# Kernel tuning notes

Measured on AMD Instinct MI355X. Metric: run time of the kernel, lower is better.

The kernel has to match this reference:

```python
import jax, jax.numpy as jnp
import numpy as np

B, S, H, E = 2, 4096, 2048, 8


def setup_inputs() -> dict:
    key = jax.random.key(0)
    k1, k2, k3 = jax.random.split(key, 3)
    x = jax.random.normal(k1, (B, S, H), dtype=jnp.float32)
    w_router = jax.random.normal(k2, (E, H), dtype=jnp.float32) * (1.0 / np.sqrt(H))
    # nn.Linear weight layout: [out_features, in_features] per expert -> [E, H, H]
    w_experts = jax.random.normal(k3, (E, H, H), dtype=jnp.float32) * (1.0 / np.sqrt(H))
    return {"x": x, "w_router": w_router, "w_experts": w_experts}


def reference(x, w_router, w_experts):
    # router logits: x @ W_r^T  -> [B, S, E]
    logits = jnp.einsum('bsh,eh->bse', x, w_router)
    idx = jnp.argmax(logits, axis=-1)  # [B, S] top-1 expert per token
    # dense all-expert outputs (matches original which evaluates every expert):
    # expert_e(x) = x @ W_e^T -> [B, S, E, H]
    all_out = jnp.einsum('bsh,efh->bsef', x, w_experts)
    # masked sum over one-hot mask == gather of the selected expert output
    out = jnp.take_along_axis(all_out, idx[:, :, None, None], axis=2)[:, :, 0, :]
    return out
```

## Files before the change

kernel.cpp:

```cpp
#include <hip/hip_runtime.h>
#include <hip/hip_bf16.h>
#include <cstdint>

#define T_TOK 8192
#define H_DIM 2048
#define N_EXP 8
#define FLAGBIT 0x80000000u

typedef __attribute__((ext_vector_type(4))) float f32x4;
typedef __attribute__((ext_vector_type(8))) short bf16x8;

__device__ __forceinline__ unsigned short f2bf(float f) {
  unsigned int u = __builtin_bit_cast(unsigned int, f);
  u += 0x7fffu + ((u >> 16) & 1u);
  return (unsigned short)(u >> 16);
}

#define GLL(SRC, DST) __builtin_amdgcn_global_load_lds( \
    (const __attribute__((address_space(1))) void*)(SRC), \
    (__attribute__((address_space(3))) void*)(DST), 16, 0, 0)

__global__ __launch_bounds__(256, 4) void k_pre(const float* __restrict__ x,
    const float* __restrict__ wr, const float* __restrict__ we,
    unsigned short* __restrict__ xb, unsigned short* __restrict__ wb,
    int* __restrict__ idx)
{
  const int bid = blockIdx.x;
  if (bid < 4096) {
    const size_t tix = ((size_t)bid * 256 + threadIdx.x) * 8;
    const size_t stride = (size_t)4096 * 256 * 8;
#pragma unroll
    for (int it = 0; it < 4; ++it) {
      const f32x4 a = *reinterpret_cast<const f32x4*>(we + tix + (size_t)it * stride);
      const f32x4 b = *reinterpret_cast<const f32x4*>(we + tix + (size_t)it * stride + 4);
      union { unsigned short h[8]; uint4 u; } r;
#pragma unroll
      for (int q = 0; q < 4; ++q) { r.h[q] = f2bf(a[q]); r.h[4 + q] = f2bf(b[q]); }
      *reinterpret_cast<uint4*>(wb + tix + (size_t)it * stride) = r.u;
    }
    return;
  }
  const int wv = threadIdx.x >> 6, lane = threadIdx.x & 63;
  const int t = (bid - 4096) * 4 + wv;
  const float* xp = x + (size_t)t * H_DIM;
  float acc[N_EXP];
#pragma unroll
  for (int e = 0; e < N_EXP; ++e) acc[e] = 0.f;
#pragma unroll
  for (int c = 0; c < H_DIM / 256; ++c) {
    const int h = c * 256 + lane * 4;
    const float4 xv = *reinterpret_cast<const float4*>(xp + h);
    ushort4 bv;
    bv.x = f2bf(xv.x); bv.y = f2bf(xv.y); bv.z = f2bf(xv.z); bv.w = f2bf(xv.w);
    *reinterpret_cast<ushort4*>(xb + (size_t)t * H_DIM + h) = bv;
#pragma unroll
    for (int e = 0; e < N_EXP; ++e) {
      const float4 wv4 = *reinterpret_cast<const float4*>(wr + e * H_DIM + h);
      acc[e] = fmaf(xv.x, wv4.x, acc[e]);
      acc[e] = fmaf(xv.y, wv4.y, acc[e]);
      acc[e] = fmaf(xv.z, wv4.z, acc[e]);
      acc[e] = fmaf(xv.w, wv4.w, acc[e]);
    }
  }
#pragma unroll
  for (int off = 32; off >= 1; off >>= 1)
#pragma unroll
    for (int e = 0; e < N_EXP; ++e) acc[e] += __shfl_xor(acc[e], off, 64);
  if (lane == 0) {
    float best = acc[0]; int be = 0;
#pragma unroll
    for (int e = 1; e < N_EXP; ++e) if (acc[e] > best) { best = acc[e]; be = e; }
    idx[t] = be;
  }
}

__global__ __launch_bounds__(1024) void k_sort(const int* __restrict__ idx,
    int* __restrict__ tlist, int* __restrict__ estar, int* __restrict__ mlo,
    int* __restrict__ mhi, int* __restrict__ rpos, int* __restrict__ rtile,
    int* __restrict__ rtc)
{
  __shared__ int wc[N_EXP][128];
  __shared__ int wbase[N_EXP][128];
  __shared__ int sTot[N_EXP];
  __shared__ int off[N_EXP + 1];
  __shared__ int sE[32], sCnt[N_EXP], sBase[N_EXP];
  const int tid = threadIdx.x, w = tid >> 6, l = tid & 63;
  int myE[8];
#pragma unroll
  for (int j = 0; j < 8; ++j) {
    myE[j] = idx[j * 1024 + tid];
#pragma unroll
    for (int e = 0; e < N_EXP; ++e) {
      const unsigned long long bm = __ballot(myE[j] == e);
      if (l == e) wc[e][j * 16 + w] = __popcll(bm);
    }
  }
  __syncthreads();
  if (tid < N_EXP) {
    int s = 0;
    for (int k = 0; k < 128; ++k) { wbase[tid][k] = s; s += wc[tid][k]; }
    sTot[tid] = s;
  }
  __syncthreads();
  if (tid == 0) {
    off[0] = 0;
    for (int e = 0; e < N_EXP; ++e) off[e + 1] = off[e] + sTot[e];
  }
  __syncthreads();
#pragma unroll
  for (int j = 0; j < 8; ++j) {
    int rank = 0;
#pragma unroll
    for (int e = 0; e < N_EXP; ++e) {
      const unsigned long long bm = __ballot(myE[j] == e);
      if (myE[j] == e) rank = __popcll(bm & ((1ull << l) - 1ull));
    }
    tlist[off[myE[j]] + wbase[myE[j]][j * 16 + w] + rank] = j * 1024 + tid;
  }
  if (tid < 32) {
    const int lo = tid * 256, hi = lo + 256;
    int bl = -1, bE = 0, bLo = 0, bHi = 0;
#pragma unroll
    for (int e = 0; e < N_EXP; ++e) {
      const int a = off[e] > lo ? off[e] : lo;
      const int b = off[e + 1] < hi ? off[e + 1] : hi;
      if (b - a > bl) { bl = b - a; bE = e; bLo = a - lo; bHi = b - lo; }
    }
    sE[tid] = bE; estar[tid] = bE; mlo[tid] = bLo; mhi[tid] = bHi;
  }
  __syncthreads();
  if (tid < N_EXP) {
    int cnt = 0;
    for (int t = 0; t < 32; ++t) {
      if (sE[t] == tid) continue;
      const int lo = t * 256, hi = lo + 256;
      const int a = off[tid] > lo ? off[tid] : lo;
      const int b = off[tid + 1] < hi ? off[tid + 1] : hi;
      if (b > a) cnt += b - a;
    }
    sCnt[tid] = cnt;
  }
  __syncthreads();
  if (tid == 0) {
    int base = 0, ntile = 0;
    for (int e = 0; e < N_EXP; ++e) {
      sBase[e] = base;
      const int pt = (sCnt[e] + 127) >> 7;
      for (int k = 0; k < pt; ++k) rtile[ntile++] = e;
      base += pt << 7;
    }
    *rtc = ntile;
  }
  __syncthreads();
  if (tid < N_EXP && sCnt[tid] > 0) {
    int ptr = sBase[tid], firstp = -1;
    for (int t = 0; t < 32; ++t) {
      if (sE[t] == tid) continue;
      const int lo = t * 256, hi = lo + 256;
      const int a = off[tid] > lo ? off[tid] : lo;
      const int b = off[tid + 1] < hi ? off[tid + 1] : hi;
      for (int p = a; p < b; ++p) { if (firstp < 0) firstp = p; rpos[ptr++] = p; }
    }
    const int end = sBase[tid] + (((sCnt[tid] + 127) >> 7) << 7);
    for (; ptr < end; ++ptr) rpos[ptr] = (int)((unsigned)firstp | FLAGBIT);
  }
}

template<int Q, bool LOADB, bool VMC>
__device__ __forceinline__ void gphase(const char* LP,
    __attribute__((address_space(3))) char* LDS3,
    int rdBase, int aRowOff, int bRowOff, int ch0, int ch1,
    bf16x8 (&bfr)[8], f32x4 (&acc)[8][4],
    const unsigned short* s0, const unsigned short* s1, int d0, int d1)
{
  if constexpr (LOADB) {
#pragma unroll
    for (int nf = 0; nf < 4; ++nf) {
      bfr[nf * 2 + 0] = *reinterpret_cast<const bf16x8*>(LP + rdBase + 32768 + bRowOff + nf * 2048 + ch0);
      bfr[nf * 2 + 1] = *reinterpret_cast<const bf16x8*>(LP + rdBase + 32768 + bRowOff + nf * 2048 + ch1);
    }
  }
  bf16x8 af[2][2];
#pragma unroll
  for (int m = 0; m < 2; ++m) {
    af[m][0] = *reinterpret_cast<const bf16x8*>(LP + rdBase + aRowOff + (2 * Q + m) * 2048 + ch0);
    af[m][1] = *reinterpret_cast<const bf16x8*>(LP + rdBase + aRowOff + (2 * Q + m) * 2048 + ch1);
  }
  GLL(s0, LDS3 + d0);
  GLL(s1, LDS3 + d1);
  __builtin_amdgcn_sched_barrier(0);
  __builtin_amdgcn_s_barrier();
  __builtin_amdgcn_sched_barrier(0);
  __builtin_amdgcn_s_setprio(1);
#pragma unroll
  for (int ks = 0; ks < 2; ++ks)
#pragma unroll
    for (int m = 0; m < 2; ++m)
#pragma unroll
      for (int nf = 0; nf < 4; ++nf)
        acc[2 * Q + m][nf] = __builtin_amdgcn_mfma_f32_16x16x32_bf16(af[m][ks], bfr[nf * 2 + ks], acc[2 * Q + m][nf], 0, 0, 0);
  __builtin_amdgcn_s_setprio(0);
  if constexpr (VMC) asm volatile("s_waitcnt vmcnt(4)" ::: "memory");
  __builtin_amdgcn_sched_barrier(0);
  __builtin_amdgcn_s_barrier();
  __builtin_amdgcn_sched_barrier(0);
}

__global__ __launch_bounds__(512, 2) void k_gemm(const unsigned short* __restrict__ xb,
    const unsigned short* __restrict__ wb, const int* __restrict__ tlist,
    const int* __restrict__ estar, const int* __restrict__ mlo, const int* __restrict__ mhi,
    const int* __restrict__ rpos, const int* __restrict__ rtile, const int* __restrict__ rtc,
    float* __restrict__ out)
{
  __shared__ short lds[65536];
  const int bid = blockIdx.x;
  const int tid = threadIdx.x;
  const int l = tid & 63, wv = tid >> 6;
  const int l16 = l & 15, g = l >> 4;
  const char* LP = (const char*)lds;
  auto* LDS3 = (__attribute__((address_space(3))) char*)lds;
  const int sw = l16 & 7;
  const int ch0 = ((0 + g) ^ sw) << 4;
  const int ch1 = ((4 + g) ^ sw) << 4;
  const int csrc = ((l & 7) ^ ((l >> 3) & 7)) * 8;
  const int srow = l >> 3;

  if (bid < 256) {
    const int mt = (bid & 7) * 4 + ((bid >> 3) & 3);
    const int nt = bid >> 5;
    const int m0 = mt * 256, f0 = nt * 256;
    const int e = estar[mt], mLo = mlo[mt], mHi = mhi[mt];
    const int wm = wv >> 2, wn = wv & 3;
    const int aRowOff = (wm * 128 + l16) * 128;
    const int bRowOff = (wn * 64 + l16) * 128;

    const unsigned short* aP[2][2];
    const unsigned short* bP[2][2];
    const unsigned short* wpan = wb + (size_t)e * H_DIM * H_DIM;
#pragma unroll
    for (int h = 0; h < 2; ++h)
#pragma unroll
      for (int j = 0; j < 2; ++j) {
        const int tok = tlist[m0 + h * 128 + (wv * 2 + j) * 8 + srow];
        aP[h][j] = xb + (size_t)tok * H_DIM + csrc;
        bP[h][j] = wpan + (size_t)(f0 + h * 128 + (wv * 2 + j) * 8 + srow) * H_DIM + csrc;
      }
    const int sl0 = wv * 2048, sl1 = wv * 2048 + 1024;

    f32x4 acc[8][4];
#pragma unroll
    for (int mf = 0; mf < 8; ++mf)
#pragma unroll
      for (int nf = 0; nf < 4; ++nf) acc[mf][nf] = (f32x4){0.f, 0.f, 0.f, 0.f};
    bf16x8 bfr[8];

    GLL(aP[0][0], LDS3 + 0 + sl0);      GLL(aP[0][1], LDS3 + 0 + sl1);
    GLL(aP[1][0], LDS3 + 16384 + sl0);  GLL(aP[1][1], LDS3 + 16384 + sl1);
    GLL(bP[0][0], LDS3 + 32768 + sl0);  GLL(bP[0][1], LDS3 + 32768 + sl1);
    GLL(bP[1][0], LDS3 + 49152 + sl0);  GLL(bP[1][1], LDS3 + 49152 + sl1);
    GLL(bP[0][0] + 64, LDS3 + 65536 + 32768 + sl0);  GLL(bP[0][1] + 64, LDS3 + 65536 + 32768 + sl1);
    GLL(bP[1][0] + 64, LDS3 + 65536 + 49152 + sl0);  GLL(bP[1][1] + 64, LDS3 + 65536 + 49152 + sl1);
    asm volatile("s_waitcnt vmcnt(4)" ::: "memory");
    __builtin_amdgcn_sched_barrier(0);
    __builtin_amdgcn_s_barrier();
    __builtin_amdgcn_sched_barrier(0);

    for (int i = 0; i < 16; ++i) {
      const int kk1 = ((2 * i + 1) << 6) & (H_DIM - 1);
      const int kk2 = ((2 * i + 2) << 6) & (H_DIM - 1);
      const int kk3 = ((2 * i + 3) << 6) & (H_DIM - 1);
      gphase<0, true , false>(LP, LDS3, 0, aRowOff, bRowOff, ch0, ch1, bfr, acc,
          aP[0][0] + kk1, aP[0][1] + kk1, 65536 + 0 + sl0, 65536 + 0 + sl1);
      gphase<1, false, false>(LP, LDS3, 0, aRowOff, bRowOff, ch0, ch1, bfr, acc,
          aP[1][0] + kk1, aP[1][1] + kk1, 65536 + 16384 + sl0, 65536 + 16384 + sl1);
      gphase<2, false, false>(LP, LDS3, 0, aRowOff, bRowOff, ch0, ch1, bfr, acc,
          bP[0][0] + kk2, bP[0][1] + kk2, 0 + 32768 + sl0, 0 + 32768 + sl1);
      gphase<3, false, true >(LP, LDS3, 0, aRowOff, bRowOff, ch0, ch1, bfr, acc,
          bP[1][0] + kk2, bP[1][1] + kk2, 0 + 49152 + sl0, 0 + 49152 + sl1);
      gphase<0, true , false>(LP, LDS3, 65536, aRowOff, bRowOff, ch0, ch1, bfr, acc,
          aP[0][0] + kk2, aP[0][1] + kk2, 0 + 0 + sl0, 0 + 0 + sl1);
      gphase<1, false, false>(LP, LDS3, 65536, aRowOff, bRowOff, ch0, ch1, bfr, acc,
          aP[1][0] + kk2, aP[1][1] + kk2, 0 + 16384 + sl0, 0 + 16384 + sl1);
      gphase<2, false, false>(LP, LDS3, 65536, aRowOff, bRowOff, ch0, ch1, bfr, acc,
          bP[0][0] + kk3, bP[0][1] + kk3, 65536 + 32768 + sl0, 65536 + 32768 + sl1);
      gphase<3, false, true >(LP, LDS3, 65536, aRowOff, bRowOff, ch0, ch1, bfr, acc,
          bP[1][0] + kk3, bP[1][1] + kk3, 65536 + 49152 + sl0, 65536 + 49152 + sl1);
    }

#pragma unroll
    for (int mf = 0; mf < 8; ++mf) {
#pragma unroll
      for (int r = 0; r < 4; ++r) {
        const int row = wm * 128 + mf * 16 + g * 4 + r;
        if (row >= mLo && row < mHi) {
          const int t = tlist[m0 + row];
          float* op = out + (size_t)t * H_DIM + f0 + wn * 64 + l16;
#pragma unroll
          for (int nf = 0; nf < 4; ++nf) op[nf * 16] = acc[mf][nf][r];
        }
      }
    }
    return;
  }

  const int bid2 = bid - 256;
  const int bx = bid2 >> 3;
  if (bx >= *rtc) return;
  const int f0 = (bid2 & 7) * 256;
  const int e = rtile[bx];
  const int wm = wv >> 2, wn = wv & 3;

  const unsigned short* aS[2];
#pragma unroll
  for (int j = 0; j < 2; ++j) {
    const int ent = rpos[bx * 128 + (wv * 2 + j) * 8 + srow];
    const int tok = tlist[ent & 0x7fffffff];
    aS[j] = xb + (size_t)tok * H_DIM + csrc;
  }
  const unsigned short* bS[4];
#pragma unroll
  for (int j = 0; j < 4; ++j)
    bS[j] = wb + (size_t)e * H_DIM * H_DIM + (size_t)(f0 + (wv * 4 + j) * 8 + srow) * H_DIM + csrc;

  f32x4 acc[4][4];
#pragma unroll
  for (int mf = 0; mf < 4; ++mf)
#pragma unroll
    for (int nf = 0; nf < 4; ++nf) acc[mf][nf] = (f32x4){0.f, 0.f, 0.f, 0.f};

  for (int it = 0; it < 32; ++it) {
    const int kk = it * 64;
    __syncthreads();
#pragma unroll
    for (int j = 0; j < 2; ++j) GLL(aS[j] + kk, LDS3 + (wv * 2 + j) * 1024);
#pragma unroll
    for (int j = 0; j < 4; ++j) GLL(bS[j] + kk, LDS3 + 16384 + (wv * 4 + j) * 1024);
    __syncthreads();
    bf16x8 af[4][2];
#pragma unroll
    for (int mf = 0; mf < 4; ++mf) {
      af[mf][0] = *reinterpret_cast<const bf16x8*>(LP + (wm * 64 + mf * 16 + l16) * 128 + ch0);
      af[mf][1] = *reinterpret_cast<const bf16x8*>(LP + (wm * 64 + mf * 16 + l16) * 128 + ch1);
    }
#pragma unroll
    for (int nf = 0; nf < 4; ++nf) {
      const bf16x8 b0 = *reinterpret_cast<const bf16x8*>(LP + 16384 + (wn * 64 + nf * 16 + l16) * 128 + ch0);
      const bf16x8 b1 = *reinterpret_cast<const bf16x8*>(LP + 16384 + (wn * 64 + nf * 16 + l16) * 128 + ch1);
#pragma unroll
      for (int mf = 0; mf < 4; ++mf) {
        acc[mf][nf] = __builtin_amdgcn_mfma_f32_16x16x32_bf16(af[mf][0], b0, acc[mf][nf], 0, 0, 0);
        acc[mf][nf] = __builtin_amdgcn_mfma_f32_16x16x32_bf16(af[mf][1], b1, acc[mf][nf], 0, 0, 0);
      }
    }
  }
#pragma unroll
  for (int mf = 0; mf < 4; ++mf) {
#pragma unroll
    for (int r = 0; r < 4; ++r) {
      const int row = wm * 64 + mf * 16 + g * 4 + r;
      const int ent = rpos[bx * 128 + row];
      if (!((unsigned)ent & FLAGBIT)) {
        const int tok = tlist[ent];
        float* op = out + (size_t)tok * H_DIM + f0 + wn * 64 + l16;
#pragma unroll
        for (int nf = 0; nf < 4; ++nf) op[nf * 16] = acc[mf][nf][r];
      }
    }
  }
}

extern "C" void kernel_launch(void* const* d_in, const int* in_sizes, int n_in,
                              void* d_out, int out_size, void* d_ws, size_t ws_size,
                              hipStream_t stream) {
  const float* x  = (const float*)d_in[0];
  const float* wr = (const float*)d_in[1];
  const float* we = (const float*)d_in[2];
  float* out = (float*)d_out;

  char* p = (char*)d_ws;
  unsigned short* xb = (unsigned short*)p; p += (size_t)T_TOK * H_DIM * 2;
  unsigned short* wb = (unsigned short*)p; p += (size_t)N_EXP * H_DIM * H_DIM * 2;
  int* idx    = (int*)p; p += T_TOK * 4;
  int* tlist  = (int*)p; p += T_TOK * 4;
  int* rpos   = (int*)p; p += T_TOK * 4;
  int* estar  = (int*)p; p += 32 * 4;
  int* mlo    = (int*)p; p += 32 * 4;
  int* mhi    = (int*)p; p += 32 * 4;
  int* rtile  = (int*)p; p += 64 * 4;
  int* rtc    = (int*)p; p += 64;

  k_pre<<<4096 + 2048, 256, 0, stream>>>(x, wr, we, xb, wb, idx);
  k_sort<<<1, 1024, 0, stream>>>(idx, tlist, estar, mlo, mhi, rpos, rtile, rtc);
  k_gemm<<<768, 512, 0, stream>>>(xb, wb, tlist, estar, mlo, mhi, rpos, rtile, rtc, out);
}
```

Measured before the change: 199.6 us.

## Split preprocessing into weight-convert and router kernels with LDS-cached router weights

Replaces the fused k_pre kernel with two launches. k_conv converts expert weights to bf16, with each thread issuing all 16 vector loads before converting so more memory requests are in flight. k_router stages the router weights in shared memory and has each wave handle four tokens, so each router-weight read is reused across tokens instead of being re-read from global memory per token. This adds a kernel launch and uses 64KB of LDS per router block, which limits occupancy.

```diff
diff --git a/kernel.cpp b/kernel.cpp
--- a/kernel.cpp
+++ b/kernel.cpp
@@ -20,57 +20,84 @@
     (const __attribute__((address_space(1))) void*)(SRC), \
     (__attribute__((address_space(3))) void*)(DST), 16, 0, 0)
 
-__global__ __launch_bounds__(256, 4) void k_pre(const float* __restrict__ x,
-    const float* __restrict__ wr, const float* __restrict__ we,
-    unsigned short* __restrict__ xb, unsigned short* __restrict__ wb,
+__global__ __launch_bounds__(256, 2) void k_conv(const float* __restrict__ we,
+                                                 unsigned short* __restrict__ wb) {
+  const size_t tix = ((size_t)blockIdx.x * 256 + threadIdx.x) * 8;
+  const size_t stride = (size_t)2048 * 256 * 8;
+  f32x4 v[16];
+#pragma unroll
+  for (int it = 0; it < 8; ++it) {
+    v[2 * it]     = *reinterpret_cast<const f32x4*>(we + tix + (size_t)it * stride);
+    v[2 * it + 1] = *reinterpret_cast<const f32x4*>(we + tix + (size_t)it * stride + 4);
+  }
+#pragma unroll
+  for (int q = 0; q < 16; ++q) asm volatile("" : "+v"(v[q]));
+#pragma unroll
+  for (int it = 0; it < 8; ++it) {
+    union { unsigned short h[8]; uint4 u; } r;
+#pragma unroll
+    for (int q = 0; q < 4; ++q) {
+      r.h[q]     = f2bf(v[2 * it][q]);
+      r.h[4 + q] = f2bf(v[2 * it + 1][q]);
+    }
+    *reinterpret_cast<uint4*>(wb + tix + (size_t)it * stride) = r.u;
+  }
+}
+
+__global__ __launch_bounds__(256) void k_router(const float* __restrict__ x,
+    const float* __restrict__ wr, unsigned short* __restrict__ xb,
     int* __restrict__ idx)
 {
-  const int bid = blockIdx.x;
-  if (bid < 4096) {
-    const size_t tix = ((size_t)bid * 256 + threadIdx.x) * 8;
-    const size_t stride = (size_t)4096 * 256 * 8;
-#pragma unroll
-    for (int it = 0; it < 4; ++it) {
-      const f32x4 a = *reinterpret_cast<const f32x4*>(we + tix + (size_t)it * stride);
-      const f32x4 b = *reinterpret_cast<const f32x4*>(we + tix + (size_t)it * stride + 4);
-      union { unsigned short h[8]; uint4 u; } r;
-#pragma unroll
-      for (int q = 0; q < 4; ++q) { r.h[q] = f2bf(a[q]); r.h[4 + q] = f2bf(b[q]); }
-      *reinterpret_cast<uint4*>(wb + tix + (size_t)it * stride) = r.u;
-    }
-    return;
-  }
+  __shared__ float swr[N_EXP * H_DIM];
+#pragma unroll
+  for (int i = 0; i < 16; ++i) {
+    const int o = (threadIdx.x + i * 256) * 4;
+    *reinterpret_cast<float4*>(&swr[o]) = *reinterpret_cast<const float4*>(&wr[o]);
+  }
+  __syncthreads();
   const int wv = threadIdx.x >> 6, lane = threadIdx.x & 63;
-  const int t = (bid - 4096) * 4 + wv;
-  const float* xp = x + (size_t)t * H_DIM;
-  float acc[N_EXP];
-#pragma unroll
-  for (int e = 0; e < N_EXP; ++e) acc[e] = 0.f;
+  const int t0 = (blockIdx.x * 4 + wv) * 4;
+  float acc[4][N_EXP];
+#pragma unroll
+  for (int tt = 0; tt < 4; ++tt)
+#pragma unroll
+    for (int e = 0; e < N_EXP; ++e) acc[tt][e] = 0.f;
 #pragma unroll
   for (int c = 0; c < H_DIM / 256; ++c) {
     const int h = c * 256 + lane * 4;
-    const float4 xv = *reinterpret_cast<const float4*>(xp + h);
-    ushort4 bv;
-    bv.x = f2bf(xv.x); bv.y = f2bf(xv.y); bv.z = f2bf(xv.z); bv.w = f2bf(xv.w);
-    *reinterpret_cast<ushort4*>(xb + (size_t)t * H_DIM + h) = bv;
-#pragma unroll
-    for (int e = 0; e < N_EXP; ++e) {
-      const float4 wv4 = *reinterpret_cast<const float4*>(wr + e * H_DIM + h);
-      acc[e] = fmaf(xv.x, wv4.x, acc[e]);
-      acc[e] = fmaf(xv.y, wv4.y, acc[e]);
-      acc[e] = fmaf(xv.z, wv4.z, acc[e]);
-      acc[e] = fmaf(xv.w, wv4.w, acc[e]);
+    float4 wvv[N_EXP];
+#pragma unroll
+    for (int e = 0; e < N_EXP; ++e)
+      wvv[e] = *reinterpret_cast<const float4*>(&swr[e * H_DIM + h]);
+#pragma unroll
+    for (int tt = 0; tt < 4; ++tt) {
+      const float4 xv = *reinterpret_cast<const float4*>(x + (size_t)(t0 + tt) * H_DIM + h);
+      ushort4 bv;
+      bv.x = f2bf(xv.x); bv.y = f2bf(xv.y); bv.z = f2bf(xv.z); bv.w = f2bf(xv.w);
+      *reinterpret_cast<ushort4*>(xb + (size_t)(t0 + tt) * H_DIM + h) = bv;
+#pragma unroll
+      for (int e = 0; e < N_EXP; ++e) {
+        acc[tt][e] = fmaf(xv.x, wvv[e].x, acc[tt][e]);
+        acc[tt][e] = fmaf(xv.y, wvv[e].y, acc[tt][e]);
+        acc[tt][e] = fmaf(xv.z, wvv[e].z, acc[tt][e]);
+        acc[tt][e] = fmaf(xv.w, wvv[e].w, acc[tt][e]);
+      }
     }
   }
 #pragma unroll
   for (int off = 32; off >= 1; off >>= 1)
 #pragma unroll
-    for (int e = 0; e < N_EXP; ++e) acc[e] += __shfl_xor(acc[e], off, 64);
+    for (int tt = 0; tt < 4; ++tt)
+#pragma unroll
+      for (int e = 0; e < N_EXP; ++e) acc[tt][e] += __shfl_xor(acc[tt][e], off, 64);
   if (lane == 0) {
-    float best = acc[0]; int be = 0;
-#pragma unroll
-    for (int e = 1; e < N_EXP; ++e) if (acc[e] > best) { best = acc[e]; be = e; }
-    idx[t] = be;
+#pragma unroll
+    for (int tt = 0; tt < 4; ++tt) {
+      float best = acc[tt][0]; int be = 0;
+#pragma unroll
+      for (int e = 1; e < N_EXP; ++e) if (acc[tt][e] > best) { best = acc[tt][e]; be = e; }
+      idx[t0 + tt] = be;
+    }
   }
 }
 
@@ -389,7 +416,8 @@
   int* rtile  = (int*)p; p += 64 * 4;
   int* rtc    = (int*)p; p += 64;
 
-  k_pre<<<4096 + 2048, 256, 0, stream>>>(x, wr, we, xb, wb, idx);
+  k_conv<<<2048, 256, 0, stream>>>(we, wb);
+  k_router<<<512, 256, 0, stream>>>(x, wr, xb, idx);
   k_sort<<<1, 1024, 0, stream>>>(idx, tlist, estar, mlo, mhi, rpos, rtile, rtc);
   k_gemm<<<768, 512, 0, stream>>>(xb, wb, tlist, estar, mlo, mhi, rpos, rtile, rtc, out);
 }
```

Result: no change. 200.1 us (+0.3%).
